# Kernel optimization log

Measured on AMD Instinct MI355X. Metric: run time of the kernel, lower is better.

The kernel has to match this reference:

```python
import jax, jax.numpy as jnp
import numpy as np

N0, N1, N2, DEG = 100000, 50000, 25000, 16
IN, HID, OUT = 256, 128, 128
H1, H2 = 2, 1
E1, E2 = N1 * DEG, N2 * DEG


def setup_inputs() -> dict:
    key = jax.random.key(0)
    ks = jax.random.split(key, 16)
    x = jax.random.normal(ks[0], (N0, IN), dtype=jnp.float32)
    # neighbor-sampled bipartite edges: each dst node has DEG sampled src neighbors
    row1 = jnp.repeat(jnp.arange(N1, dtype=jnp.int32), DEG)
    col1 = jax.random.randint(ks[1], (E1,), 0, N0, dtype=jnp.int32)
    t1 = jax.random.randint(ks[2], (E1,), 0, 100, dtype=jnp.int32)
    row2 = jnp.repeat(jnp.arange(N2, dtype=jnp.int32), DEG)
    col2 = jax.random.randint(ks[3], (E2,), 0, N1, dtype=jnp.int32)
    t2 = jax.random.randint(ks[4], (E2,), 0, 100, dtype=jnp.int32)
    s_in = 1.0 / np.sqrt(IN)
    s_h = 1.0 / np.sqrt(HID)
    s_bn = 1.0 / np.sqrt(HID * H1)
    return dict(
        x=x, row1=row1, col1=col1, t1=t1, row2=row2, col2=col2, t2=t2,
        time=10, interval=20,
        Ws1=jax.random.normal(ks[5], (IN, H1 * HID), jnp.float32) * s_in,
        Wd1=jax.random.normal(ks[6], (IN, H1 * HID), jnp.float32) * s_in,
        as1=jax.random.normal(ks[7], (H1, HID), jnp.float32) * s_h,
        ad1=jax.random.normal(ks[8], (H1, HID), jnp.float32) * s_h,
        b1=jnp.zeros((H1 * HID,), jnp.float32),
        g1=jnp.ones((H1 * HID,), jnp.float32),
        beta1=jnp.zeros((H1 * HID,), jnp.float32),
        m1=jnp.zeros((H1 * HID,), jnp.float32),
        v1=jnp.ones((H1 * HID,), jnp.float32),
        Ws2=jax.random.normal(ks[9], (H1 * HID, H2 * OUT), jnp.float32) * s_bn,
        Wd2=jax.random.normal(ks[10], (H1 * HID, H2 * OUT), jnp.float32) * s_bn,
        as2=jax.random.normal(ks[11], (H2, OUT), jnp.float32) * s_h,
        ad2=jax.random.normal(ks[12], (H2, OUT), jnp.float32) * s_h,
        b2=jnp.zeros((H2 * OUT,), jnp.float32),
    )


def gat_conv(hs, hd, row, col, mask, att_s, att_d, n_dst):
    # hs: [Ns,H,C] transformed src feats, hd: [Nd,H,C]; row=dst idx, col=src idx per edge
    a_s = jnp.sum(hs * att_s, axis=-1)  # [Ns,H]
    a_d = jnp.sum(hd * att_d, axis=-1)  # [Nd,H]
    e = jax.nn.leaky_relu(a_s[col] + a_d[row], negative_slope=0.2)  # [E,H]
    e = jnp.where(mask[:, None], e, -jnp.inf)
    m = jax.ops.segment_max(e, row, num_segments=n_dst)  # [Nd,H]
    m = jnp.where(jnp.isfinite(m), m, 0.0)
    ex = jnp.where(mask[:, None], jnp.exp(e - m[row]), 0.0)
    denom = jax.ops.segment_sum(ex, row, num_segments=n_dst)
    alpha = ex / jnp.maximum(denom[row], 1e-16)  # edge softmax over incoming edges
    out = jax.ops.segment_sum(alpha[:, :, None] * hs[col], row, num_segments=n_dst)
    return out  # [Nd,H,C]


def _forward(x, Ws1, Wd1, as1, ad1, b1, g1, beta1, m1, v1,
             Ws2, Wd2, as2, ad2, b2,
             row1, col1, t1, row2, col2, t2, time, interval):
    # temporal edge masking: keep edges with timestamp in [time, time+interval)
    mask1 = (t1 >= time) & (t1 < time + interval)
    mask2 = (t2 >= time) & (t2 < time + interval)
    # ---- layer 1: GATConv(IN -> HID, heads=H1, concat=True) ----
    hs = (x @ Ws1).reshape(N0, H1, HID)
    hd = (x[:N1] @ Wd1).reshape(N1, H1, HID)
    h = gat_conv(hs, hd, row1, col1, mask1, as1, ad1, N1).reshape(N1, H1 * HID) + b1
    # BatchNorm1d (eval: running stats), then leaky_relu (slope 0.01); dropout off (eval)
    h = (h - m1) * jax.lax.rsqrt(v1 + 1e-5) * g1 + beta1
    h = jax.nn.leaky_relu(h, negative_slope=0.01)
    # ---- layer 2: GATConv(H1*HID -> OUT, heads=H2, concat=False) ----
    hs2 = (h @ Ws2).reshape(N1, H2, OUT)
    hd2 = (h[:N2] @ Wd2).reshape(N2, H2, OUT)
    out = gat_conv(hs2, hd2, row2, col2, mask2, as2, ad2, N2)
    out = jnp.mean(out, axis=1) + b2  # concat=False -> mean over heads
    return out  # [N2, OUT]


def reference(x, row1, col1, t1, row2, col2, t2, time, interval,
              Ws1, Wd1, as1, ad1, b1, g1, beta1, m1, v1,
              Ws2, Wd2, as2, ad2, b2):
    return _forward(x, Ws1, Wd1, as1, ad1, b1, g1, beta1, m1, v1,
                    Ws2, Wd2, as2, ad2, b2,
                    row1, col1, t1, row2, col2, t2, time, interval)
```

## Files before the change

kernel.cpp:

```cpp
#include <hip/hip_runtime.h>
#include <hip/hip_bf16.h>

#define N0C 100000
#define N1C 50000
#define N2C 25000

typedef _Float16 f16;
typedef _Float16 f16x2 __attribute__((ext_vector_type(2)));
typedef _Float16 f16x4 __attribute__((ext_vector_type(4)));
typedef _Float16 f16x8 __attribute__((ext_vector_type(8)));
typedef float f32x16 __attribute__((ext_vector_type(16)));

typedef const __attribute__((address_space(1))) unsigned int guint;
typedef __attribute__((address_space(3))) unsigned int luint;
__device__ __forceinline__ void gload16(const void* g, void* l) {
    __builtin_amdgcn_global_load_lds((guint*)g, (luint*)l, 16, 0, 0);
}

__global__ void prep1_kernel(const float* __restrict__ Ws1, const float* __restrict__ Wd1,
                             const float* __restrict__ as1, const float* __restrict__ ad1,
                             const float* __restrict__ Ws2, const float* __restrict__ Wd2,
                             const float* __restrict__ as2, const float* __restrict__ ad2,
                             const float* __restrict__ b1, const float* __restrict__ g1,
                             const float* __restrict__ beta1, const float* __restrict__ m1,
                             const float* __restrict__ v1,
                             float* __restrict__ e1, float* __restrict__ e2,
                             float* __restrict__ bns, float* __restrict__ bnt) {
    int k = blockIdx.x, lane = threadIdx.x;
    float s0 = 0, s1 = 0, d0 = 0, d1 = 0, t0 = 0, t1 = 0;
    for (int c = lane; c < 128; c += 64) {
        s0 += Ws1[k * 256 + c] * as1[c];
        s1 += Ws1[k * 256 + 128 + c] * as1[128 + c];
        d0 += Wd1[k * 256 + c] * ad1[c];
        d1 += Wd1[k * 256 + 128 + c] * ad1[128 + c];
        t0 += Ws2[k * 128 + c] * as2[c];
        t1 += Wd2[k * 128 + c] * ad2[c];
    }
    for (int d = 1; d < 64; d <<= 1) {
        s0 += __shfl_xor(s0, d); s1 += __shfl_xor(s1, d);
        d0 += __shfl_xor(d0, d); d1 += __shfl_xor(d1, d);
        t0 += __shfl_xor(t0, d); t1 += __shfl_xor(t1, d);
    }
    if (lane == 0) {
        e1[k * 4 + 0] = s0; e1[k * 4 + 1] = s1; e1[k * 4 + 2] = d0; e1[k * 4 + 3] = d1;
        e2[k * 2 + 0] = t0; e2[k * 2 + 1] = t1;
        float sc = g1[k] * rsqrtf(v1[k] + 1e-5f);
        bns[k] = sc;
        bnt[k] = (b1[k] - m1[k]) * sc + beta1[k];
    }
}

__global__ void prep2_kernel(const float* __restrict__ Ws1, const float* __restrict__ Ws2,
                             const float* __restrict__ e1, const float* __restrict__ e2,
                             f16* __restrict__ bfl1, f16* __restrict__ bfl2) {
    int i = blockIdx.x * 256 + threadIdx.x;
    if (i < 73728) {
        int j = i & 7, lane = (i >> 3) & 63, kb = (i >> 9) & 15, nt = i >> 13;
        int c = lane & 31, hi = lane >> 5;
        int k = kb * 16 + hi * 8 + j;
        float v;
        if (nt < 8) v = Ws1[k * 256 + nt * 32 + c];
        else v = (c < 4) ? e1[k * 4 + c] : 0.f;
        bfl1[i] = (f16)v;
    } else {
        int i2 = i - 73728;
        if (i2 < 40960) {
            int j = i2 & 7, lane = (i2 >> 3) & 63, kb = (i2 >> 9) & 15, nt = i2 >> 13;
            int c = lane & 31, hi = lane >> 5;
            int k = kb * 16 + hi * 8 + j;
            float v;
            if (nt < 4) v = Ws2[k * 128 + nt * 32 + c];
            else v = (c < 2) ? e2[k * 2 + c] : 0.f;
            bfl2[i2] = (f16)v;
        }
    }
}

__global__ __launch_bounds__(512, 4) void gemm1_kernel(
    const float* __restrict__ x, const f16* __restrict__ bfl,
    f16* __restrict__ hs, float* __restrict__ as_out, float* __restrict__ ad_out) {
    __shared__ __align__(16) unsigned char smA[16384];
    __shared__ __align__(16) unsigned char smB[36864];
    const int t = threadIdx.x;
    const int wave = t >> 6, lane = t & 63;
    const int wr = wave & 3, wg = wave >> 2;
    const int col = lane & 31, hi = lane >> 5;
    const int r0 = blockIdx.x * 128;

    const int arow = t >> 2, aq = t & 3;
    const int agrow = r0 + arow;
    const int asw_st = (arow & 7) << 4;
    const bool aval = agrow < N0C;
    const float4* abase = (const float4*)(x + (size_t)agrow * 256);

    f32x16 acc[5] = {};

    for (int s = 0; s < 4; s++) {
        for (int c = wave; c < 36; c += 8) {
            int nt = c >> 2, kbl = c & 3;
            const f16* src = bfl + ((size_t)(nt * 16 + s * 4 + kbl) * 64 + lane) * 8;
            gload16(src, smB + c * 1024);
        }
        {
            float4 a0, a1, a2, a3;
            if (aval) {
                const float4* p = abase + s * 16 + aq * 4;
                a0 = p[0]; a1 = p[1]; a2 = p[2]; a3 = p[3];
            } else {
                a0 = make_float4(0.f, 0.f, 0.f, 0.f);
                a1 = a0; a2 = a0; a3 = a0;
            }
            f16x8 v0 = {(f16)a0.x, (f16)a0.y, (f16)a0.z, (f16)a0.w,
                        (f16)a1.x, (f16)a1.y, (f16)a1.z, (f16)a1.w};
            f16x8 v1 = {(f16)a2.x, (f16)a2.y, (f16)a2.z, (f16)a2.w,
                        (f16)a3.x, (f16)a3.y, (f16)a3.z, (f16)a3.w};
            unsigned char* wb = smA + arow * 128;
            *(f16x8*)(wb + ((aq * 32) ^ asw_st)) = v0;
            *(f16x8*)(wb + ((aq * 32 + 16) ^ asw_st)) = v1;
        }
        __syncthreads();
        const int myrow = wr * 32 + col;
        const int asw = (myrow & 7) << 4;
        const int abyte = myrow * 128 + hi * 16;
        if (wg == 0) {
#pragma unroll
            for (int kb = 0; kb < 4; kb++) {
                f16x8 af = *(const f16x8*)(smA + ((abyte + kb * 32) ^ asw));
#pragma unroll
                for (int j = 0; j < 5; j++) {
                    f16x8 bf = *(const f16x8*)(smB + (j * 4 + kb) * 1024 + lane * 16);
                    acc[j] = __builtin_amdgcn_mfma_f32_32x32x16_f16(af, bf, acc[j], 0, 0, 0);
                }
            }
        } else {
#pragma unroll
            for (int kb = 0; kb < 4; kb++) {
                f16x8 af = *(const f16x8*)(smA + ((abyte + kb * 32) ^ asw));
#pragma unroll
                for (int j = 0; j < 4; j++) {
                    f16x8 bf = *(const f16x8*)(smB + ((5 + j) * 4 + kb) * 1024 + lane * 16);
                    acc[j] = __builtin_amdgcn_mfma_f32_32x32x16_f16(af, bf, acc[j], 0, 0, 0);
                }
            }
        }
        __syncthreads();
    }

    const int rbase = r0 + wr * 32 + 4 * hi;
    if (wg == 0) {
#pragma unroll
        for (int j = 0; j < 5; j++)
#pragma unroll
            for (int r = 0; r < 16; r++) {
                int grow = rbase + (r & 3) + 8 * (r >> 2);
                if (grow < N0C) hs[(size_t)grow * 256 + j * 32 + col] = (f16)acc[j][r];
            }
    } else {
#pragma unroll
        for (int j = 0; j < 3; j++)
#pragma unroll
            for (int r = 0; r < 16; r++) {
                int grow = rbase + (r & 3) + 8 * (r >> 2);
                if (grow < N0C) hs[(size_t)grow * 256 + (5 + j) * 32 + col] = (f16)acc[j][r];
            }
#pragma unroll
        for (int r = 0; r < 16; r++) {
            int grow = rbase + (r & 3) + 8 * (r >> 2);
            float v = acc[3][r];
            if (col < 2) {
                if (grow < N0C) as_out[grow * 2 + col] = v;
            } else if (col < 4) {
                if (grow < N1C) ad_out[grow * 2 + (col - 2)] = v;
            }
        }
    }
}

__global__ __launch_bounds__(512, 4) void gemm2_kernel(
    const f16* __restrict__ h, const f16* __restrict__ bfl,
    f16* __restrict__ hs2, float* __restrict__ as_out, float* __restrict__ ad_out) {
    __shared__ __align__(16) unsigned char smA[16384];
    __shared__ __align__(16) unsigned char smB[20480];
    const int t = threadIdx.x;
    const int wave = t >> 6, lane = t & 63;
    const int wr = wave & 3, wg = wave >> 2;
    const int col = lane & 31, hi = lane >> 5;
    const int r0 = blockIdx.x * 128;

    const int arow_l = lane >> 3;
    const int agr = (lane & 7) ^ arow_l;

    f32x16 acc[3] = {};

    for (int s = 0; s < 4; s++) {
        for (int c = wave; c < 36; c += 8) {
            if (c < 16) {
                int rl = c * 8 + arow_l;
                int rsrc = r0 + rl;
                if (rsrc > N1C - 1) rsrc = N1C - 1;
                const f16* src = h + (size_t)rsrc * 256 + s * 64 + agr * 8;
                gload16(src, smA + c * 1024);
            } else {
                int c2 = c - 16;
                int nt = c2 >> 2, kbl = c2 & 3;
                const f16* src = bfl + ((size_t)(nt * 16 + s * 4 + kbl) * 64 + lane) * 8;
                gload16(src, smB + c2 * 1024);
            }
        }
        __syncthreads();
        const int myrow = wr * 32 + col;
        const int asw = (myrow & 7) << 4;
        const int abyte = myrow * 128 + hi * 16;
        if (wg == 0) {
#pragma unroll
            for (int kb = 0; kb < 4; kb++) {
                f16x8 af = *(const f16x8*)(smA + ((abyte + kb * 32) ^ asw));
#pragma unroll
                for (int j = 0; j < 3; j++) {
                    f16x8 bf = *(const f16x8*)(smB + (j * 4 + kb) * 1024 + lane * 16);
                    acc[j] = __builtin_amdgcn_mfma_f32_32x32x16_f16(af, bf, acc[j], 0, 0, 0);
                }
            }
        } else {
#pragma unroll
            for (int kb = 0; kb < 4; kb++) {
                f16x8 af = *(const f16x8*)(smA + ((abyte + kb * 32) ^ asw));
#pragma unroll
                for (int j = 0; j < 2; j++) {
                    f16x8 bf = *(const f16x8*)(smB + ((3 + j) * 4 + kb) * 1024 + lane * 16);
                    acc[j] = __builtin_amdgcn_mfma_f32_32x32x16_f16(af, bf, acc[j], 0, 0, 0);
                }
            }
        }
        __syncthreads();
    }

    const int rbase = r0 + wr * 32 + 4 * hi;
    if (wg == 0) {
#pragma unroll
        for (int j = 0; j < 3; j++)
#pragma unroll
            for (int r = 0; r < 16; r++) {
                int grow = rbase + (r & 3) + 8 * (r >> 2);
                if (grow < N1C) hs2[(size_t)grow * 128 + j * 32 + col] = (f16)acc[j][r];
            }
    } else {
#pragma unroll
        for (int r = 0; r < 16; r++) {
            int grow = rbase + (r & 3) + 8 * (r >> 2);
            if (grow < N1C) hs2[(size_t)grow * 128 + 3 * 32 + col] = (f16)acc[0][r];
        }
#pragma unroll
        for (int r = 0; r < 16; r++) {
            int grow = rbase + (r & 3) + 8 * (r >> 2);
            float v = acc[1][r];
            if (col == 0) {
                if (grow < N1C) as_out[grow] = v;
            } else if (col == 1) {
                if (grow < N2C) ad_out[grow] = v;
            }
        }
    }
}

__global__ void agg1_kernel(const int* __restrict__ col1, const int* __restrict__ t1,
                            const int* __restrict__ timep, const int* __restrict__ intervalp,
                            const float* __restrict__ a_s, const float* __restrict__ a_d,
                            const f16* __restrict__ hs,
                            const float* __restrict__ bns, const float* __restrict__ bnt,
                            f16* __restrict__ h) {
    int wid = (blockIdx.x * blockDim.x + threadIdx.x) >> 6;
    if (wid >= N1C) return;
    int lane = threadIdx.x & 63;
    int T = timep[0], I = intervalp[0];
    int j = lane & 15;
    int c = col1[wid * 16 + j];
    int tv = t1[wid * 16 + j];
    bool mk = (tv >= T) && (tv < T + I);
    float e0 = -INFINITY, e1 = -INFINITY;
    if (mk) {
        float s0 = a_s[c * 2 + 0] + a_d[wid * 2 + 0];
        float s1 = a_s[c * 2 + 1] + a_d[wid * 2 + 1];
        e0 = s0 > 0.f ? s0 : 0.2f * s0;
        e1 = s1 > 0.f ? s1 : 0.2f * s1;
    }
    float m0 = e0, m1 = e1;
#pragma unroll
    for (int d = 1; d < 16; d <<= 1) {
        m0 = fmaxf(m0, __shfl_xor(m0, d));
        m1 = fmaxf(m1, __shfl_xor(m1, d));
    }
    float ex0 = mk ? __expf(e0 - m0) : 0.f;
    float ex1 = mk ? __expf(e1 - m1) : 0.f;
    float s0 = ex0, s1 = ex1;
#pragma unroll
    for (int d = 1; d < 16; d <<= 1) {
        s0 += __shfl_xor(s0, d);
        s1 += __shfl_xor(s1, d);
    }
    float r0 = 1.f / fmaxf(s0, 1e-16f);
    float r1 = 1.f / fmaxf(s1, 1e-16f);
    unsigned long long mb = __ballot(mk) & 0xFFFFull;
    int head = lane >> 5;
    float rden = head ? r1 : r0;
    float acc0 = 0.f, acc1 = 0.f, acc2 = 0.f, acc3 = 0.f;
    while (mb) {
        int jj = __builtin_ctzll(mb);
        mb &= mb - 1;
        int cj = __shfl(c, jj);
        float w0 = __shfl(ex0, jj), w1 = __shfl(ex1, jj);
        float w = (head ? w1 : w0) * rden;
        f16x4 v = *(const f16x4*)(hs + (size_t)cj * 256 + lane * 4);
        acc0 += w * (float)v[0];
        acc1 += w * (float)v[1];
        acc2 += w * (float)v[2];
        acc3 += w * (float)v[3];
    }
    int cb = lane * 4;
    float4 sc = *(const float4*)(bns + cb);
    float4 sh = *(const float4*)(bnt + cb);
    float o0 = acc0 * sc.x + sh.x; o0 = o0 > 0.f ? o0 : 0.01f * o0;
    float o1 = acc1 * sc.y + sh.y; o1 = o1 > 0.f ? o1 : 0.01f * o1;
    float o2 = acc2 * sc.z + sh.z; o2 = o2 > 0.f ? o2 : 0.01f * o2;
    float o3 = acc3 * sc.w + sh.w; o3 = o3 > 0.f ? o3 : 0.01f * o3;
    f16x4 ov = {(f16)o0, (f16)o1, (f16)o2, (f16)o3};
    *(f16x4*)(h + (size_t)wid * 256 + cb) = ov;
}

__global__ void agg2_kernel(const int* __restrict__ col2, const int* __restrict__ t2,
                            const int* __restrict__ timep, const int* __restrict__ intervalp,
                            const float* __restrict__ a_s, const float* __restrict__ a_d,
                            const f16* __restrict__ hs2,
                            const float* __restrict__ b2, float* __restrict__ out) {
    int wid = (blockIdx.x * blockDim.x + threadIdx.x) >> 6;
    if (wid >= N2C) return;
    int lane = threadIdx.x & 63;
    int T = timep[0], I = intervalp[0];
    int j = lane & 15;
    int c = col2[wid * 16 + j];
    int tv = t2[wid * 16 + j];
    bool mk = (tv >= T) && (tv < T + I);
    float e = -INFINITY;
    if (mk) {
        float s = a_s[c] + a_d[wid];
        e = s > 0.f ? s : 0.2f * s;
    }
    float m = e;
#pragma unroll
    for (int d = 1; d < 16; d <<= 1) m = fmaxf(m, __shfl_xor(m, d));
    float ex = mk ? __expf(e - m) : 0.f;
    float s = ex;
#pragma unroll
    for (int d = 1; d < 16; d <<= 1) s += __shfl_xor(s, d);
    float r = 1.f / fmaxf(s, 1e-16f);
    unsigned long long mb = __ballot(mk) & 0xFFFFull;
    float acc0 = 0.f, acc1 = 0.f;
    while (mb) {
        int jj = __builtin_ctzll(mb);
        mb &= mb - 1;
        int cj = __shfl(c, jj);
        float w = __shfl(ex, jj) * r;
        f16x2 v = *(const f16x2*)(hs2 + (size_t)cj * 128 + lane * 2);
        acc0 += w * (float)v[0];
        acc1 += w * (float)v[1];
    }
    float2 o = make_float2(acc0 + b2[lane * 2], acc1 + b2[lane * 2 + 1]);
    *(float2*)(out + (size_t)wid * 128 + lane * 2) = o;
}

extern "C" void kernel_launch(void* const* d_in, const int* in_sizes, int n_in,
                              void* d_out, int out_size, void* d_ws, size_t ws_size,
                              hipStream_t stream) {
    const float* x = (const float*)d_in[0];
    const int* col1 = (const int*)d_in[2];
    const int* t1 = (const int*)d_in[3];
    const int* col2 = (const int*)d_in[5];
    const int* t2 = (const int*)d_in[6];
    const int* timep = (const int*)d_in[7];
    const int* intervalp = (const int*)d_in[8];
    const float* Ws1 = (const float*)d_in[9];
    const float* Wd1 = (const float*)d_in[10];
    const float* as1 = (const float*)d_in[11];
    const float* ad1 = (const float*)d_in[12];
    const float* b1 = (const float*)d_in[13];
    const float* g1 = (const float*)d_in[14];
    const float* beta1 = (const float*)d_in[15];
    const float* m1 = (const float*)d_in[16];
    const float* v1 = (const float*)d_in[17];
    const float* Ws2 = (const float*)d_in[18];
    const float* Wd2 = (const float*)d_in[19];
    const float* as2 = (const float*)d_in[20];
    const float* ad2 = (const float*)d_in[21];
    const float* b2 = (const float*)d_in[22];
    float* out = (float*)d_out;

    char* ws = (char*)d_ws;
    size_t off = 0;
    auto alloc = [&](size_t bytes) {
        size_t o = off;
        off += (bytes + 511) & ~(size_t)511;
        return o;
    };
    f16* hs = (f16*)(ws + alloc((size_t)N0C * 256 * 2));
    f16* h = (f16*)(ws + alloc((size_t)N1C * 256 * 2));
    f16* hs2 = (f16*)(ws + alloc((size_t)N1C * 128 * 2));
    float* a_s1 = (float*)(ws + alloc((size_t)N0C * 2 * 4));
    float* a_d1 = (float*)(ws + alloc((size_t)N1C * 2 * 4));
    float* a_s2 = (float*)(ws + alloc((size_t)N1C * 4));
    float* a_d2 = (float*)(ws + alloc((size_t)N2C * 4));
    f16* bfl1 = (f16*)(ws + alloc((size_t)73728 * 2));
    f16* bfl2 = (f16*)(ws + alloc((size_t)40960 * 2));
    float* e1 = (float*)(ws + alloc(1024 * 4));
    float* e2 = (float*)(ws + alloc(512 * 4));
    float* bns = (float*)(ws + alloc(256 * 4));
    float* bnt = (float*)(ws + alloc(256 * 4));

    prep1_kernel<<<256, 64, 0, stream>>>(Ws1, Wd1, as1, ad1, Ws2, Wd2, as2, ad2,
                                         b1, g1, beta1, m1, v1, e1, e2, bns, bnt);
    prep2_kernel<<<448, 256, 0, stream>>>(Ws1, Ws2, e1, e2, bfl1, bfl2);
    gemm1_kernel<<<(N0C + 127) / 128, 512, 0, stream>>>(x, bfl1, hs, a_s1, a_d1);
    agg1_kernel<<<N1C / 4, 256, 0, stream>>>(col1, t1, timep, intervalp,
                                             a_s1, a_d1, hs, bns, bnt, h);
    gemm2_kernel<<<(N1C + 127) / 128, 512, 0, stream>>>(h, bfl2, hs2, a_s2, a_d2);
    agg2_kernel<<<N2C / 4, 256, 0, stream>>>(col2, t2, timep, intervalp,
                                             a_s2, a_d2, hs2, b2, out);
}
```

Measured before the change: 101.2 us.

## Load full-K A tile to LDS once and stream B fragments from global

Both GEMM kernels now load the entire 64-row by 256-K A tile into shared memory in one pass with a single barrier, instead of four K-stages with two barriers each. B fragments are read directly from global memory (cached, small weight buffer) rather than staged through LDS with global_load_lds. Blocks shrink to 256 threads and 64 rows, doubling the grid. The aim is to remove per-stage synchronisation and B staging. In exchange, B reads go through L1/L2 with per-wave latency and there is no overlap between loading A and the MFMA work.

```diff
diff --git a/kernel.cpp b/kernel.cpp
--- a/kernel.cpp
+++ b/kernel.cpp
@@ -10,12 +10,6 @@
 typedef _Float16 f16x4 __attribute__((ext_vector_type(4)));
 typedef _Float16 f16x8 __attribute__((ext_vector_type(8)));
 typedef float f32x16 __attribute__((ext_vector_type(16)));
-
-typedef const __attribute__((address_space(1))) unsigned int guint;
-typedef __attribute__((address_space(3))) unsigned int luint;
-__device__ __forceinline__ void gload16(const void* g, void* l) {
-    __builtin_amdgcn_global_load_lds((guint*)g, (luint*)l, 16, 0, 0);
-}
 
 __global__ void prep1_kernel(const float* __restrict__ Ws1, const float* __restrict__ Wd1,
                              const float* __restrict__ as1, const float* __restrict__ ad1,
@@ -76,78 +70,49 @@
     }
 }
 
-__global__ __launch_bounds__(512, 4) void gemm1_kernel(
+__global__ __launch_bounds__(256, 4) void gemm1_kernel(
     const float* __restrict__ x, const f16* __restrict__ bfl,
     f16* __restrict__ hs, float* __restrict__ as_out, float* __restrict__ ad_out) {
-    __shared__ __align__(16) unsigned char smA[16384];
-    __shared__ __align__(16) unsigned char smB[36864];
+    __shared__ __align__(16) unsigned char smA[32768];
     const int t = threadIdx.x;
     const int wave = t >> 6, lane = t & 63;
-    const int wr = wave & 3, wg = wave >> 2;
+    const int wr = wave & 1, wg = wave >> 1;
     const int col = lane & 31, hi = lane >> 5;
-    const int r0 = blockIdx.x * 128;
-
-    const int arow = t >> 2, aq = t & 3;
-    const int agrow = r0 + arow;
-    const int asw_st = (arow & 7) << 4;
-    const bool aval = agrow < N0C;
-    const float4* abase = (const float4*)(x + (size_t)agrow * 256);
-
-    f32x16 acc[5] = {};
-
-    for (int s = 0; s < 4; s++) {
-        for (int c = wave; c < 36; c += 8) {
-            int nt = c >> 2, kbl = c & 3;
-            const f16* src = bfl + ((size_t)(nt * 16 + s * 4 + kbl) * 64 + lane) * 8;
-            gload16(src, smB + c * 1024);
-        }
-        {
-            float4 a0, a1, a2, a3;
-            if (aval) {
-                const float4* p = abase + s * 16 + aq * 4;
-                a0 = p[0]; a1 = p[1]; a2 = p[2]; a3 = p[3];
-            } else {
-                a0 = make_float4(0.f, 0.f, 0.f, 0.f);
-                a1 = a0; a2 = a0; a3 = a0;
-            }
-            f16x8 v0 = {(f16)a0.x, (f16)a0.y, (f16)a0.z, (f16)a0.w,
-                        (f16)a1.x, (f16)a1.y, (f16)a1.z, (f16)a1.w};
-            f16x8 v1 = {(f16)a2.x, (f16)a2.y, (f16)a2.z, (f16)a2.w,
-                        (f16)a3.x, (f16)a3.y, (f16)a3.z, (f16)a3.w};
-            unsigned char* wb = smA + arow * 128;
-            *(f16x8*)(wb + ((aq * 32) ^ asw_st)) = v0;
-            *(f16x8*)(wb + ((aq * 32 + 16) ^ asw_st)) = v1;
-        }
-        __syncthreads();
-        const int myrow = wr * 32 + col;
-        const int asw = (myrow & 7) << 4;
-        const int abyte = myrow * 128 + hi * 16;
-        if (wg == 0) {
-#pragma unroll
-            for (int kb = 0; kb < 4; kb++) {
-                f16x8 af = *(const f16x8*)(smA + ((abyte + kb * 32) ^ asw));
-#pragma unroll
-                for (int j = 0; j < 5; j++) {
-                    f16x8 bf = *(const f16x8*)(smB + (j * 4 + kb) * 1024 + lane * 16);
-                    acc[j] = __builtin_amdgcn_mfma_f32_32x32x16_f16(af, bf, acc[j], 0, 0, 0);
-                }
-            }
-        } else {
-#pragma unroll
-            for (int kb = 0; kb < 4; kb++) {
-                f16x8 af = *(const f16x8*)(smA + ((abyte + kb * 32) ^ asw));
-#pragma unroll
-                for (int j = 0; j < 4; j++) {
-                    f16x8 bf = *(const f16x8*)(smB + ((5 + j) * 4 + kb) * 1024 + lane * 16);
-                    acc[j] = __builtin_amdgcn_mfma_f32_32x32x16_f16(af, bf, acc[j], 0, 0, 0);
-                }
-            }
-        }
-        __syncthreads();
-    }
-
+    const int r0 = blockIdx.x * 64;
+
+    {
+        int arow = t >> 2, q = t & 3;
+        int grow = r0 + arow;
+        int sw = (arow & 7) << 4;
+        const float4* src = (const float4*)(x + (size_t)grow * 256) + q * 16;
+        unsigned char* wb = smA + arow * 512;
+#pragma unroll
+        for (int i = 0; i < 8; i++) {
+            float4 a0, a1;
+            if (grow < N0C) { a0 = src[2 * i]; a1 = src[2 * i + 1]; }
+            else { a0 = make_float4(0.f, 0.f, 0.f, 0.f); a1 = a0; }
+            f16x8 v = {(f16)a0.x, (f16)a0.y, (f16)a0.z, (f16)a0.w,
+                       (f16)a1.x, (f16)a1.y, (f16)a1.z, (f16)a1.w};
+            *(f16x8*)(wb + ((q * 128 + i * 16) ^ sw)) = v;
+        }
+    }
+    __syncthreads();
+
+    const int myrow = wr * 32 + col;
+    const int asw = (myrow & 7) << 4;
+    const int abase = myrow * 512 + hi * 16;
     const int rbase = r0 + wr * 32 + 4 * hi;
+
     if (wg == 0) {
+        f32x16 acc[5] = {};
+        for (int kb = 0; kb < 16; kb++) {
+            f16x8 af = *(const f16x8*)(smA + ((abase + kb * 32) ^ asw));
+#pragma unroll
+            for (int j = 0; j < 5; j++) {
+                f16x8 bf = *(const f16x8*)(bfl + ((size_t)(j * 16 + kb) * 64 + lane) * 8);
+                acc[j] = __builtin_amdgcn_mfma_f32_32x32x16_f16(af, bf, acc[j], 0, 0, 0);
+            }
+        }
 #pragma unroll
         for (int j = 0; j < 5; j++)
 #pragma unroll
@@ -156,6 +121,15 @@
                 if (grow < N0C) hs[(size_t)grow * 256 + j * 32 + col] = (f16)acc[j][r];
             }
     } else {
+        f32x16 acc[4] = {};
+        for (int kb = 0; kb < 16; kb++) {
+            f16x8 af = *(const f16x8*)(smA + ((abase + kb * 32) ^ asw));
+#pragma unroll
+            for (int j = 0; j < 4; j++) {
+                f16x8 bf = *(const f16x8*)(bfl + ((size_t)((5 + j) * 16 + kb) * 64 + lane) * 8);
+                acc[j] = __builtin_amdgcn_mfma_f32_32x32x16_f16(af, bf, acc[j], 0, 0, 0);
+            }
+        }
 #pragma unroll
         for (int j = 0; j < 3; j++)
 #pragma unroll
@@ -176,67 +150,47 @@
     }
 }
 
-__global__ __launch_bounds__(512, 4) void gemm2_kernel(
+__global__ __launch_bounds__(256, 4) void gemm2_kernel(
     const f16* __restrict__ h, const f16* __restrict__ bfl,
     f16* __restrict__ hs2, float* __restrict__ as_out, float* __restrict__ ad_out) {
-    __shared__ __align__(16) unsigned char smA[16384];
-    __shared__ __align__(16) unsigned char smB[20480];
+    __shared__ __align__(16) unsigned char smA[32768];
     const int t = threadIdx.x;
     const int wave = t >> 6, lane = t & 63;
-    const int wr = wave & 3, wg = wave >> 2;
+    const int wr = wave & 1, wg = wave >> 1;
     const int col = lane & 31, hi = lane >> 5;
-    const int r0 = blockIdx.x * 128;
-
-    const int arow_l = lane >> 3;
-    const int agr = (lane & 7) ^ arow_l;
-
-    f32x16 acc[3] = {};
-
-    for (int s = 0; s < 4; s++) {
-        for (int c = wave; c < 36; c += 8) {
-            if (c < 16) {
-                int rl = c * 8 + arow_l;
-                int rsrc = r0 + rl;
-                if (rsrc > N1C - 1) rsrc = N1C - 1;
-                const f16* src = h + (size_t)rsrc * 256 + s * 64 + agr * 8;
-                gload16(src, smA + c * 1024);
-            } else {
-                int c2 = c - 16;
-                int nt = c2 >> 2, kbl = c2 & 3;
-                const f16* src = bfl + ((size_t)(nt * 16 + s * 4 + kbl) * 64 + lane) * 8;
-                gload16(src, smB + c2 * 1024);
-            }
-        }
-        __syncthreads();
-        const int myrow = wr * 32 + col;
-        const int asw = (myrow & 7) << 4;
-        const int abyte = myrow * 128 + hi * 16;
-        if (wg == 0) {
-#pragma unroll
-            for (int kb = 0; kb < 4; kb++) {
-                f16x8 af = *(const f16x8*)(smA + ((abyte + kb * 32) ^ asw));
-#pragma unroll
-                for (int j = 0; j < 3; j++) {
-                    f16x8 bf = *(const f16x8*)(smB + (j * 4 + kb) * 1024 + lane * 16);
-                    acc[j] = __builtin_amdgcn_mfma_f32_32x32x16_f16(af, bf, acc[j], 0, 0, 0);
-                }
-            }
-        } else {
-#pragma unroll
-            for (int kb = 0; kb < 4; kb++) {
-                f16x8 af = *(const f16x8*)(smA + ((abyte + kb * 32) ^ asw));
-#pragma unroll
-                for (int j = 0; j < 2; j++) {
-                    f16x8 bf = *(const f16x8*)(smB + ((3 + j) * 4 + kb) * 1024 + lane * 16);
-                    acc[j] = __builtin_amdgcn_mfma_f32_32x32x16_f16(af, bf, acc[j], 0, 0, 0);
-                }
-            }
-        }
-        __syncthreads();
-    }
-
+    const int r0 = blockIdx.x * 64;
+
+    {
+        int arow = t >> 2, q = t & 3;
+        int grow = r0 + arow;
+        int sw = (arow & 7) << 4;
+        const unsigned char* src = (const unsigned char*)(h + (size_t)grow * 256) + q * 128;
+        unsigned char* wb = smA + arow * 512;
+#pragma unroll
+        for (int i = 0; i < 8; i++) {
+            int4 v;
+            if (grow < N1C) v = *(const int4*)(src + i * 16);
+            else v = make_int4(0, 0, 0, 0);
+            *(int4*)(wb + ((q * 128 + i * 16) ^ sw)) = v;
+        }
+    }
+    __syncthreads();
+
+    const int myrow = wr * 32 + col;
+    const int asw = (myrow & 7) << 4;
+    const int abase = myrow * 512 + hi * 16;
     const int rbase = r0 + wr * 32 + 4 * hi;
+
     if (wg == 0) {
+        f32x16 acc[3] = {};
+        for (int kb = 0; kb < 16; kb++) {
+            f16x8 af = *(const f16x8*)(smA + ((abase + kb * 32) ^ asw));
+#pragma unroll
+            for (int j = 0; j < 3; j++) {
+                f16x8 bf = *(const f16x8*)(bfl + ((size_t)(j * 16 + kb) * 64 + lane) * 8);
+                acc[j] = __builtin_amdgcn_mfma_f32_32x32x16_f16(af, bf, acc[j], 0, 0, 0);
+            }
+        }
 #pragma unroll
         for (int j = 0; j < 3; j++)
 #pragma unroll
@@ -245,6 +199,15 @@
                 if (grow < N1C) hs2[(size_t)grow * 128 + j * 32 + col] = (f16)acc[j][r];
             }
     } else {
+        f32x16 acc[2] = {};
+        for (int kb = 0; kb < 16; kb++) {
+            f16x8 af = *(const f16x8*)(smA + ((abase + kb * 32) ^ asw));
+#pragma unroll
+            for (int j = 0; j < 2; j++) {
+                f16x8 bf = *(const f16x8*)(bfl + ((size_t)((3 + j) * 16 + kb) * 64 + lane) * 8);
+                acc[j] = __builtin_amdgcn_mfma_f32_32x32x16_f16(af, bf, acc[j], 0, 0, 0);
+            }
+        }
 #pragma unroll
         for (int r = 0; r < 16; r++) {
             int grow = rbase + (r & 3) + 8 * (r >> 2);
@@ -418,10 +381,10 @@
     prep1_kernel<<<256, 64, 0, stream>>>(Ws1, Wd1, as1, ad1, Ws2, Wd2, as2, ad2,
                                          b1, g1, beta1, m1, v1, e1, e2, bns, bnt);
     prep2_kernel<<<448, 256, 0, stream>>>(Ws1, Ws2, e1, e2, bfl1, bfl2);
-    gemm1_kernel<<<(N0C + 127) / 128, 512, 0, stream>>>(x, bfl1, hs, a_s1, a_d1);
+    gemm1_kernel<<<(N0C + 63) / 64, 256, 0, stream>>>(x, bfl1, hs, a_s1, a_d1);
     agg1_kernel<<<N1C / 4, 256, 0, stream>>>(col1, t1, timep, intervalp,
                                              a_s1, a_d1, hs, bns, bnt, h);
-    gemm2_kernel<<<(N1C + 127) / 128, 512, 0, stream>>>(h, bfl2, hs2, a_s2, a_d2);
+    gemm2_kernel<<<(N1C + 63) / 64, 256, 0, stream>>>(h, bfl2, hs2, a_s2, a_d2);
     agg2_kernel<<<N2C / 4, 256, 0, stream>>>(col2, t2, timep, intervalp,
                                              a_s2, a_d2, hs2, b2, out);
 }
```

Measured after the change: 131.8 us. 30.3% more time.

## Double-buffer LDS in both GEMM kernels and store A in MFMA fragment order

Applied to the files above, without the earlier changes.

Both GEMM kernels now work through K in 8 chunks of 32 instead of 4 chunks of 64, using two LDS buffers. Loads for the next chunk are issued before the MFMAs on the current chunk so memory latency overlaps compute, leaving one barrier per chunk instead of two. A tiles are written in MFMA fragment order, which removes the XOR swizzle and lets each lane read its A fragment contiguously. The cost is twice as many loop iterations and barriers at a smaller tile depth, plus extra registers to hold prefetched A values in gemm1.

```diff
diff --git a/kernel.cpp b/kernel.cpp
--- a/kernel.cpp
+++ b/kernel.cpp
@@ -15,6 +15,11 @@
 typedef __attribute__((address_space(3))) unsigned int luint;
 __device__ __forceinline__ void gload16(const void* g, void* l) {
     __builtin_amdgcn_global_load_lds((guint*)g, (luint*)l, 16, 0, 0);
+}
+
+__device__ __forceinline__ f16x8 cvt8(float4 a, float4 b) {
+    return (f16x8){(f16)a.x, (f16)a.y, (f16)a.z, (f16)a.w,
+                   (f16)b.x, (f16)b.y, (f16)b.z, (f16)b.w};
 }
 
 __global__ void prep1_kernel(const float* __restrict__ Ws1, const float* __restrict__ Wd1,
@@ -79,8 +84,8 @@
 __global__ __launch_bounds__(512, 4) void gemm1_kernel(
     const float* __restrict__ x, const f16* __restrict__ bfl,
     f16* __restrict__ hs, float* __restrict__ as_out, float* __restrict__ ad_out) {
-    __shared__ __align__(16) unsigned char smA[16384];
-    __shared__ __align__(16) unsigned char smB[36864];
+    __shared__ __align__(16) unsigned char smA[2][8192];
+    __shared__ __align__(16) unsigned char smB[2][18432];
     const int t = threadIdx.x;
     const int wave = t >> 6, lane = t & 63;
     const int wr = wave & 3, wg = wave >> 2;
@@ -88,61 +93,54 @@
     const int r0 = blockIdx.x * 128;
 
     const int arow = t >> 2, aq = t & 3;
-    const int agrow = r0 + arow;
-    const int asw_st = (arow & 7) << 4;
-    const bool aval = agrow < N0C;
-    const float4* abase = (const float4*)(x + (size_t)agrow * 256);
+    const int grow_a = r0 + arow;
+    const bool aval = grow_a < N0C;
+    const float4* abase = (const float4*)(x + (size_t)grow_a * 256);
+    const int aslot = (((arow >> 5) * 2 + (aq >> 1)) * 64 + (aq & 1) * 32 + (arow & 31)) * 16;
+
+    float4 a0, a1;
+    if (aval) { a0 = abase[aq * 2]; a1 = abase[aq * 2 + 1]; }
+    else { a0 = make_float4(0.f, 0.f, 0.f, 0.f); a1 = a0; }
+    for (int c = wave; c < 18; c += 8) {
+        int nt = c >> 1, kbl = c & 1;
+        gload16(bfl + ((size_t)(nt * 16 + kbl) * 64 + lane) * 8, smB[0] + c * 1024 + lane * 16);
+    }
+    *(f16x8*)(smA[0] + aslot) = cvt8(a0, a1);
+    __syncthreads();
 
     f32x16 acc[5] = {};
-
-    for (int s = 0; s < 4; s++) {
-        for (int c = wave; c < 36; c += 8) {
-            int nt = c >> 2, kbl = c & 3;
-            const f16* src = bfl + ((size_t)(nt * 16 + s * 4 + kbl) * 64 + lane) * 8;
-            gload16(src, smB + c * 1024);
-        }
-        {
-            float4 a0, a1, a2, a3;
+    for (int ch = 0; ch < 8; ch++) {
+        const int cur = ch & 1, nxt = cur ^ 1;
+        const bool pre = ch < 7;
+        if (pre) {
             if (aval) {
-                const float4* p = abase + s * 16 + aq * 4;
-                a0 = p[0]; a1 = p[1]; a2 = p[2]; a3 = p[3];
-            } else {
-                a0 = make_float4(0.f, 0.f, 0.f, 0.f);
-                a1 = a0; a2 = a0; a3 = a0;
-            }
-            f16x8 v0 = {(f16)a0.x, (f16)a0.y, (f16)a0.z, (f16)a0.w,
-                        (f16)a1.x, (f16)a1.y, (f16)a1.z, (f16)a1.w};
-            f16x8 v1 = {(f16)a2.x, (f16)a2.y, (f16)a2.z, (f16)a2.w,
-                        (f16)a3.x, (f16)a3.y, (f16)a3.z, (f16)a3.w};
-            unsigned char* wb = smA + arow * 128;
-            *(f16x8*)(wb + ((aq * 32) ^ asw_st)) = v0;
-            *(f16x8*)(wb + ((aq * 32 + 16) ^ asw_st)) = v1;
-        }
-        __syncthreads();
-        const int myrow = wr * 32 + col;
-        const int asw = (myrow & 7) << 4;
-        const int abyte = myrow * 128 + hi * 16;
-        if (wg == 0) {
-#pragma unroll
-            for (int kb = 0; kb < 4; kb++) {
-                f16x8 af = *(const f16x8*)(smA + ((abyte + kb * 32) ^ asw));
+                const float4* p = abase + (ch + 1) * 8 + aq * 2;
+                a0 = p[0]; a1 = p[1];
+            }
+            for (int c = wave; c < 18; c += 8) {
+                int nt = c >> 1, kbl = c & 1;
+                gload16(bfl + ((size_t)(nt * 16 + (ch + 1) * 2 + kbl) * 64 + lane) * 8,
+                        smB[nxt] + c * 1024 + lane * 16);
+            }
+        }
+#pragma unroll
+        for (int kb = 0; kb < 2; kb++) {
+            f16x8 af = *(const f16x8*)(smA[cur] + ((wr * 2 + kb) * 64 + lane) * 16);
+            if (wg == 0) {
 #pragma unroll
                 for (int j = 0; j < 5; j++) {
-                    f16x8 bf = *(const f16x8*)(smB + (j * 4 + kb) * 1024 + lane * 16);
+                    f16x8 bf = *(const f16x8*)(smB[cur] + (j * 2 + kb) * 1024 + lane * 16);
                     acc[j] = __builtin_amdgcn_mfma_f32_32x32x16_f16(af, bf, acc[j], 0, 0, 0);
                 }
-            }
-        } else {
-#pragma unroll
-            for (int kb = 0; kb < 4; kb++) {
-                f16x8 af = *(const f16x8*)(smA + ((abyte + kb * 32) ^ asw));
+            } else {
 #pragma unroll
                 for (int j = 0; j < 4; j++) {
-                    f16x8 bf = *(const f16x8*)(smB + ((5 + j) * 4 + kb) * 1024 + lane * 16);
+                    f16x8 bf = *(const f16x8*)(smB[cur] + ((5 + j) * 2 + kb) * 1024 + lane * 16);
                     acc[j] = __builtin_amdgcn_mfma_f32_32x32x16_f16(af, bf, acc[j], 0, 0, 0);
                 }
             }
         }
+        if (pre) *(f16x8*)(smA[nxt] + aslot) = cvt8(a0, a1);
         __syncthreads();
     }
 
@@ -179,55 +177,51 @@
 __global__ __launch_bounds__(512, 4) void gemm2_kernel(
     const f16* __restrict__ h, const f16* __restrict__ bfl,
     f16* __restrict__ hs2, float* __restrict__ as_out, float* __restrict__ ad_out) {
-    __shared__ __align__(16) unsigned char smA[16384];
-    __shared__ __align__(16) unsigned char smB[20480];
+    __shared__ __align__(16) unsigned char smA[2][8192];
+    __shared__ __align__(16) unsigned char smB[2][10240];
     const int t = threadIdx.x;
     const int wave = t >> 6, lane = t & 63;
     const int wr = wave & 3, wg = wave >> 2;
     const int col = lane & 31, hi = lane >> 5;
     const int r0 = blockIdx.x * 128;
 
-    const int arow_l = lane >> 3;
-    const int agr = (lane & 7) ^ arow_l;
+    const int wrA = wave >> 1, kbA = wave & 1;
+    int arowg = r0 + wrA * 32 + col;
+    if (arowg > N1C - 1) arowg = N1C - 1;
+    const f16* asrc = h + (size_t)arowg * 256 + kbA * 16 + hi * 8;
+
+    gload16(asrc, smA[0] + wave * 1024 + lane * 16);
+    for (int c = wave; c < 10; c += 8) {
+        int nt = c >> 1, kbl = c & 1;
+        gload16(bfl + ((size_t)(nt * 16 + kbl) * 64 + lane) * 8, smB[0] + c * 1024 + lane * 16);
+    }
+    __syncthreads();
 
     f32x16 acc[3] = {};
-
-    for (int s = 0; s < 4; s++) {
-        for (int c = wave; c < 36; c += 8) {
-            if (c < 16) {
-                int rl = c * 8 + arow_l;
-                int rsrc = r0 + rl;
-                if (rsrc > N1C - 1) rsrc = N1C - 1;
-                const f16* src = h + (size_t)rsrc * 256 + s * 64 + agr * 8;
-                gload16(src, smA + c * 1024);
-            } else {
-                int c2 = c - 16;
-                int nt = c2 >> 2, kbl = c2 & 3;
-                const f16* src = bfl + ((size_t)(nt * 16 + s * 4 + kbl) * 64 + lane) * 8;
-                gload16(src, smB + c2 * 1024);
-            }
-        }
-        __syncthreads();
-        const int myrow = wr * 32 + col;
-        const int asw = (myrow & 7) << 4;
-        const int abyte = myrow * 128 + hi * 16;
-        if (wg == 0) {
-#pragma unroll
-            for (int kb = 0; kb < 4; kb++) {
-                f16x8 af = *(const f16x8*)(smA + ((abyte + kb * 32) ^ asw));
+    for (int ch = 0; ch < 8; ch++) {
+        const int cur = ch & 1, nxt = cur ^ 1;
+        const bool pre = ch < 7;
+        if (pre) {
+            gload16(asrc + (ch + 1) * 32, smA[nxt] + wave * 1024 + lane * 16);
+            for (int c = wave; c < 10; c += 8) {
+                int nt = c >> 1, kbl = c & 1;
+                gload16(bfl + ((size_t)(nt * 16 + (ch + 1) * 2 + kbl) * 64 + lane) * 8,
+                        smB[nxt] + c * 1024 + lane * 16);
+            }
+        }
+#pragma unroll
+        for (int kb = 0; kb < 2; kb++) {
+            f16x8 af = *(const f16x8*)(smA[cur] + ((wr * 2 + kb) * 64 + lane) * 16);
+            if (wg == 0) {
 #pragma unroll
                 for (int j = 0; j < 3; j++) {
-                    f16x8 bf = *(const f16x8*)(smB + (j * 4 + kb) * 1024 + lane * 16);
+                    f16x8 bf = *(const f16x8*)(smB[cur] + (j * 2 + kb) * 1024 + lane * 16);
                     acc[j] = __builtin_amdgcn_mfma_f32_32x32x16_f16(af, bf, acc[j], 0, 0, 0);
                 }
-            }
-        } else {
-#pragma unroll
-            for (int kb = 0; kb < 4; kb++) {
-                f16x8 af = *(const f16x8*)(smA + ((abyte + kb * 32) ^ asw));
+            } else {
 #pragma unroll
                 for (int j = 0; j < 2; j++) {
-                    f16x8 bf = *(const f16x8*)(smB + ((3 + j) * 4 + kb) * 1024 + lane * 16);
+                    f16x8 bf = *(const f16x8*)(smB[cur] + ((3 + j) * 2 + kb) * 1024 + lane * 16);
                     acc[j] = __builtin_amdgcn_mfma_f32_32x32x16_f16(af, bf, acc[j], 0, 0, 0);
                 }
             }
```

After: 103.7 us. +2.5%, slower.
